# Performance work log

Measured on AMD Instinct MI355X. Metric: run time of the kernel, lower is better.

Reference implementation:

```python
import jax, jax.numpy as jnp
import numpy as np

EMBED_DIM = 1024
NUM_HEADS = 16
HEAD_DIM = EMBED_DIM // NUM_HEADS


def setup_inputs() -> dict:
    key = jax.random.key(0)
    k1, k2, k3, k4, k5 = jax.random.split(key, 5)
    B, N, C = 8, 1024, EMBED_DIM
    s = 1.0 / np.sqrt(C)
    return {
        "x": jax.random.normal(k1, (B, N, C), dtype=jnp.float32),
        "in_proj_weight": jax.random.normal(k2, (3 * C, C), dtype=jnp.float32) * s,
        "in_proj_bias": jax.random.normal(k3, (3 * C,), dtype=jnp.float32) * 0.02,
        "out_proj_weight": jax.random.normal(k4, (C, C), dtype=jnp.float32) * s,
        "out_proj_bias": jax.random.normal(k5, (C,), dtype=jnp.float32) * 0.02,
    }


def reference(x, in_proj_weight, in_proj_bias, out_proj_weight, out_proj_bias):
    B, N, C = x.shape
    scale = HEAD_DIM ** -0.5
    # qkv projection: F.linear(x, W, b) = x @ W.T + b -> [B, N, 3C]
    qkv = jnp.einsum("bnc,dc->bnd", x, in_proj_weight) + in_proj_bias
    # [B, N, 3, H, Dh] -> [3, B, H, N, Dh]
    qkv = qkv.reshape(B, N, 3, NUM_HEADS, HEAD_DIM).transpose(2, 0, 3, 1, 4)
    q, k, v = qkv[0], qkv[1], qkv[2]
    attn = jnp.einsum("bhqd,bhkd->bhqk", q, k) * scale
    attn = jax.nn.softmax(attn, axis=-1)
    out = jnp.einsum("bhqk,bhkd->bhqd", attn, v)
    out = out.transpose(0, 2, 1, 3).reshape(B, N, C)
    return jnp.einsum("bnc,dc->bnd", out, out_proj_weight) + out_proj_bias
```

## Files before the change

kernel.cpp:

```cpp
#include <hip/hip_runtime.h>
#include <math.h>
#include <stdint.h>

#define SEQ   1024
#define BATCH 8
#define CDIM  1024
#define HEADS 16
#define DHEAD 64

typedef __bf16 bf16;
typedef _Float16 f16;
typedef __attribute__((ext_vector_type(8))) _Float16 f16x8;
typedef __attribute__((ext_vector_type(4))) float f32x4;

static __device__ __forceinline__ void gl16(const void* g, void* l) {
    __builtin_amdgcn_global_load_lds(
        (const __attribute__((address_space(1))) void*)(uintptr_t)g,
        (__attribute__((address_space(3))) void*)(uintptr_t)l,
        16, 0, 0);
}

__global__ __launch_bounds__(256)
void cvt_f16(const float* __restrict__ in, f16* __restrict__ out, int n8)
{
    int i = blockIdx.x * blockDim.x + threadIdx.x;
    const int stride = gridDim.x * blockDim.x;
    for (; i < n8; i += stride) {
        const f32x4 v0 = *(const f32x4*)(in + (size_t)i * 8);
        const f32x4 v1 = *(const f32x4*)(in + (size_t)i * 8 + 4);
        f16x8 o;
#pragma unroll
        for (int j = 0; j < 4; j++) {
            o[j]     = (f16)v0[j];
            o[j + 4] = (f16)v1[j];
        }
        *(f16x8*)(out + (size_t)i * 8) = o;
    }
}

template<int MODE>
__global__ __launch_bounds__(256, 3)
void gemm_f16(const f16* __restrict__ Ag, const f16* __restrict__ Bg,
              const float* __restrict__ bias, float* __restrict__ out0,
              f16* __restrict__ qg, f16* __restrict__ kgp, f16* __restrict__ vgp,
              int M, int Ncols, int K)
{
    __shared__ f16 As[3][4][128][8];
    __shared__ f16 Bs[3][4][128][8];

    const int m0   = blockIdx.y * 128;
    const int n0   = blockIdx.x * 128;

    const int tid  = threadIdx.x;
    const int wid  = tid >> 6;
    const int lane = tid & 63;
    const int wr   = (wid >> 1) * 64;
    const int wc   = (wid & 1) * 64;
    const int l16  = lane & 15;
    const int kgf  = lane >> 4;

    const int kg0 = tid >> 7, row0 = tid & 127;
    const f16* aP = Ag + (size_t)(m0 + row0) * K + kg0 * 8;
    const f16* bP = Bg + (size_t)(n0 + row0) * K + kg0 * 8;
    const int loff = wid << 10;

#define STAGE(buf, kt)                                              \
    do {                                                            \
        gl16(aP + (kt),      (char*)&As[buf][0][0][0] + loff);      \
        gl16(aP + (kt) + 16, (char*)&As[buf][0][0][0] + loff + 4096);\
        gl16(bP + (kt),      (char*)&Bs[buf][0][0][0] + loff);      \
        gl16(bP + (kt) + 16, (char*)&Bs[buf][0][0][0] + loff + 4096);\
    } while (0)

#define COMPUTE(buf)                                                        \
    do {                                                                    \
        f16x8 fa[4], fb[4];                                                 \
        _Pragma("unroll")                                                   \
        for (int i = 0; i < 4; i++) {                                       \
            fa[i] = *(const f16x8*)&As[buf][kgf][wr + i * 16 + l16][0];     \
            fb[i] = *(const f16x8*)&Bs[buf][kgf][wc + i * 16 + l16][0];     \
        }                                                                   \
        _Pragma("unroll")                                                   \
        for (int mi = 0; mi < 4; mi++)                                      \
            _Pragma("unroll")                                               \
            for (int ni = 0; ni < 4; ni++)                                  \
                acc[mi][ni] = __builtin_amdgcn_mfma_f32_16x16x32_f16(       \
                    fa[mi], fb[ni], acc[mi][ni], 0, 0, 0);                  \
    } while (0)

    f32x4 acc[4][4];
#pragma unroll
    for (int i = 0; i < 4; i++)
#pragma unroll
        for (int j = 0; j < 4; j++) acc[i][j] = (f32x4)0.f;

    const int T = K >> 5;

    STAGE(0, 0);
    STAGE(1, 32);

    int cur = 0;
    for (int t = 0; t < T - 2; t++) {
        const int nbuf = (cur == 0) ? 2 : (cur - 1);
        STAGE(nbuf, (t + 2) << 5);
        asm volatile("s_waitcnt vmcnt(8)" ::: "memory");
        __builtin_amdgcn_sched_barrier(0);
        __builtin_amdgcn_s_barrier();
        __builtin_amdgcn_sched_barrier(0);
        COMPUTE(cur);
        __builtin_amdgcn_sched_barrier(0);
        __builtin_amdgcn_s_barrier();
        cur = (cur == 2) ? 0 : (cur + 1);
    }

    asm volatile("s_waitcnt vmcnt(4)" ::: "memory");
    __builtin_amdgcn_sched_barrier(0);
    __builtin_amdgcn_s_barrier();
    __builtin_amdgcn_sched_barrier(0);
    COMPUTE(cur);
    __builtin_amdgcn_sched_barrier(0);
    __builtin_amdgcn_s_barrier();
    cur = (cur == 2) ? 0 : (cur + 1);

    asm volatile("s_waitcnt vmcnt(0)" ::: "memory");
    __builtin_amdgcn_sched_barrier(0);
    __builtin_amdgcn_s_barrier();
    __builtin_amdgcn_sched_barrier(0);
    COMPUTE(cur);

#undef STAGE
#undef COMPUTE

#pragma unroll
    for (int ni = 0; ni < 4; ni++) {
        const int d  = n0 + wc + ni * 16 + l16;
        const float bv = bias[d];
        int s = 0, hh = 0, dh = 0;
        if (MODE == 1) {
            s  = d >> 10;
            hh = (d >> 6) & 15;
            dh = d & 63;
        }
#pragma unroll
        for (int mi = 0; mi < 4; mi++) {
            const int mbase = m0 + wr + mi * 16 + (lane >> 4) * 4;
#pragma unroll
            for (int r = 0; r < 4; r++) {
                const float v = acc[mi][ni][r] + bv;
                const int m = mbase + r;
                if (MODE == 0) {
                    out0[(size_t)m * Ncols + d] = v;
                } else {
                    const int b = m >> 10, n = m & 1023;
                    const size_t bho = (size_t)((b << 4) + hh) << 16;
                    if (s == 0)
                        qg[bho + ((size_t)n << 6) + dh] = (f16)(v * 0.125f);
                    else if (s == 1)
                        kgp[bho + ((size_t)n << 6) + dh] = (f16)v;
                    else
                        vgp[bho + ((size_t)dh << 10) + n] = (f16)v;
                }
            }
        }
    }
    (void)M;
}

__global__ __launch_bounds__(256, 4)
void attn_mfma(const f16* __restrict__ qf, const f16* __restrict__ kf,
               const f16* __restrict__ vtf, f16* __restrict__ og)
{
    __shared__ f16 Kl[8][64][8];
    __shared__ f16 Vl[8][64][8];
    __shared__ f16 Pl[4][16][72];

    const int tid  = threadIdx.x;
    const int wid  = tid >> 6;
    const int lane = tid & 63;
    const int l16  = lane & 15;
    const int kg   = lane >> 4;
    const int bh   = blockIdx.y;
    const int q0   = blockIdx.x << 6;

    const size_t bhoff = (size_t)bh << 16;
    const f16* qb = qf  + bhoff;
    const f16* kb = kf  + bhoff;
    const f16* vb = vtf + bhoff;

    f16x8 qfr[2];
    {
        const f16* qrow = qb + ((size_t)(q0 + wid * 16 + l16) << 6);
        qfr[0] = *(const f16x8*)(qrow + kg * 8);
        qfr[1] = *(const f16x8*)(qrow + 32 + kg * 8);
    }

    const int c0 = tid,        col0 = c0 & 63, slot0 = c0 >> 6;
    const int c1 = tid + 256,  col1 = c1 & 63, slot1 = c1 >> 6;

    float mrow[4], lrow[4];
    f32x4 accO[4];
#pragma unroll
    for (int r = 0; r < 4; r++) { mrow[r] = -INFINITY; lrow[r] = 0.f; }
#pragma unroll
    for (int t = 0; t < 4; t++) accO[t] = (f32x4)0.f;

    f16x8 rk0 = *(const f16x8*)(kb + ((size_t)col0 << 6) + slot0 * 8);
    f16x8 rk1 = *(const f16x8*)(kb + ((size_t)col1 << 6) + slot1 * 8);
    f16x8 rv0 = *(const f16x8*)(vb + ((size_t)col0 << 10) + slot0 * 8);
    f16x8 rv1 = *(const f16x8*)(vb + ((size_t)col1 << 10) + slot1 * 8);

    for (int kt = 0; kt < 16; kt++) {
        __syncthreads();
        *(f16x8*)&Kl[slot0][col0][0] = rk0;
        *(f16x8*)&Kl[slot1][col1][0] = rk1;
        *(f16x8*)&Vl[slot0][col0][0] = rv0;
        *(f16x8*)&Vl[slot1][col1][0] = rv1;
        __syncthreads();

        if (kt < 15) {
            const int n1 = (kt + 1) << 6;
            rk0 = *(const f16x8*)(kb + ((size_t)(n1 + col0) << 6) + slot0 * 8);
            rk1 = *(const f16x8*)(kb + ((size_t)(n1 + col1) << 6) + slot1 * 8);
            rv0 = *(const f16x8*)(vb + ((size_t)col0 << 10) + n1 + slot0 * 8);
            rv1 = *(const f16x8*)(vb + ((size_t)col1 << 10) + n1 + slot1 * 8);
        }

        f32x4 accS[4];
#pragma unroll
        for (int t = 0; t < 4; t++) accS[t] = (f32x4)0.f;
#pragma unroll
        for (int t = 0; t < 4; t++) {
            const f16x8 kf0 = *(const f16x8*)&Kl[kg][t * 16 + l16][0];
            const f16x8 kf1 = *(const f16x8*)&Kl[4 + kg][t * 16 + l16][0];
            accS[t] = __builtin_amdgcn_mfma_f32_16x16x32_f16(qfr[0], kf0, accS[t], 0, 0, 0);
            accS[t] = __builtin_amdgcn_mfma_f32_16x16x32_f16(qfr[1], kf1, accS[t], 0, 0, 0);
        }

#pragma unroll
        for (int r = 0; r < 4; r++) {
            float sm = fmaxf(fmaxf(accS[0][r], accS[1][r]),
                             fmaxf(accS[2][r], accS[3][r]));
            sm = fmaxf(sm, __shfl_xor(sm, 1, 16));
            sm = fmaxf(sm, __shfl_xor(sm, 2, 16));
            sm = fmaxf(sm, __shfl_xor(sm, 4, 16));
            sm = fmaxf(sm, __shfl_xor(sm, 8, 16));
            const float mn = fmaxf(mrow[r], sm);
            const float al = __expf(mrow[r] - mn);
            float p0 = __expf(accS[0][r] - mn);
            float p1 = __expf(accS[1][r] - mn);
            float p2 = __expf(accS[2][r] - mn);
            float p3 = __expf(accS[3][r] - mn);
            float rs = (p0 + p1) + (p2 + p3);
            rs += __shfl_xor(rs, 1, 16);
            rs += __shfl_xor(rs, 2, 16);
            rs += __shfl_xor(rs, 4, 16);
            rs += __shfl_xor(rs, 8, 16);
            lrow[r] = lrow[r] * al + rs;
            mrow[r] = mn;
            accO[0][r] *= al;
            accO[1][r] *= al;
            accO[2][r] *= al;
            accO[3][r] *= al;
            const int prow = kg * 4 + r;
            Pl[wid][prow][l16]      = (f16)p0;
            Pl[wid][prow][16 + l16] = (f16)p1;
            Pl[wid][prow][32 + l16] = (f16)p2;
            Pl[wid][prow][48 + l16] = (f16)p3;
        }

#pragma unroll
        for (int h = 0; h < 2; h++) {
            const f16x8 pa = *(const f16x8*)&Pl[wid][l16][h * 32 + kg * 8];
#pragma unroll
            for (int t = 0; t < 4; t++) {
                const f16x8 vf = *(const f16x8*)&Vl[h * 4 + kg][t * 16 + l16][0];
                accO[t] = __builtin_amdgcn_mfma_f32_16x16x32_f16(pa, vf, accO[t], 0, 0, 0);
            }
        }
    }

    const int b = bh >> 4, hh = bh & 15;
#pragma unroll
    for (int r = 0; r < 4; r++) {
        const float inv = 1.0f / lrow[r];
        const int n = q0 + wid * 16 + kg * 4 + r;
        const size_t base = ((((size_t)b << 10) + n) << 10) + hh * 64;
#pragma unroll
        for (int t = 0; t < 4; t++)
            og[base + t * 16 + l16] = (f16)(accO[t][r] * inv);
    }
}

#define TILE 128
#define KB   16
#define LSTR (TILE + 4)

template<int MODE>
__global__ __launch_bounds__(256, 2)
void gemm_bt(const float* __restrict__ A, const float* __restrict__ Bm,
             const float* __restrict__ bias, float* __restrict__ out0,
             float* __restrict__ qg, float* __restrict__ kg, float* __restrict__ vg,
             int M, int Ncols, int K)
{
    __shared__ float As[KB][LSTR];
    __shared__ float Bs[KB][LSTR];

    const int tid = threadIdx.x;
    const int tr  = tid >> 4;
    const int tc  = tid & 15;
    const int m0  = blockIdx.y * TILE;
    const int n0  = blockIdx.x * TILE;

    const int lrow = tid >> 2;
    const int lcol = (tid & 3) << 2;

    const float* Ap = A  + (size_t)(m0 + lrow) * K + lcol;
    const float* Bp = Bm + (size_t)(n0 + lrow) * K + lcol;
    const size_t rstep = (size_t)64 * K;

    float acc[8][8];
#pragma unroll
    for (int i = 0; i < 8; i++)
#pragma unroll
        for (int j = 0; j < 8; j++) acc[i][j] = 0.f;

    for (int kt = 0; kt < K; kt += KB) {
        float4 a0 = *(const float4*)(Ap + kt);
        float4 a1 = *(const float4*)(Ap + rstep + kt);
        float4 b0 = *(const float4*)(Bp + kt);
        float4 b1 = *(const float4*)(Bp + rstep + kt);
        __syncthreads();
        As[lcol + 0][lrow]      = a0.x;
        As[lcol + 1][lrow]      = a0.y;
        As[lcol + 2][lrow]      = a0.z;
        As[lcol + 3][lrow]      = a0.w;
        As[lcol + 0][lrow + 64] = a1.x;
        As[lcol + 1][lrow + 64] = a1.y;
        As[lcol + 2][lrow + 64] = a1.z;
        As[lcol + 3][lrow + 64] = a1.w;
        Bs[lcol + 0][lrow]      = b0.x;
        Bs[lcol + 1][lrow]      = b0.y;
        Bs[lcol + 2][lrow]      = b0.z;
        Bs[lcol + 3][lrow]      = b0.w;
        Bs[lcol + 0][lrow + 64] = b1.x;
        Bs[lcol + 1][lrow + 64] = b1.y;
        Bs[lcol + 2][lrow + 64] = b1.z;
        Bs[lcol + 3][lrow + 64] = b1.w;
        __syncthreads();
#pragma unroll
        for (int kk = 0; kk < KB; kk++) {
            float ar[8], br[8];
            *(float4*)&ar[0] = *(const float4*)&As[kk][tr << 2];
            *(float4*)&ar[4] = *(const float4*)&As[kk][64 + (tr << 2)];
            *(float4*)&br[0] = *(const float4*)&Bs[kk][tc << 2];
            *(float4*)&br[4] = *(const float4*)&Bs[kk][64 + (tc << 2)];
#pragma unroll
            for (int i = 0; i < 8; i++)
#pragma unroll
                for (int j = 0; j < 8; j++)
                    acc[i][j] = fmaf(ar[i], br[j], acc[i][j]);
        }
    }

#pragma unroll
    for (int rg = 0; rg < 2; rg++) {
#pragma unroll
        for (int ri = 0; ri < 4; ri++) {
            const int m = m0 + rg * 64 + (tr << 2) + ri;
#pragma unroll
            for (int cg = 0; cg < 2; cg++) {
                const int d = n0 + cg * 64 + (tc << 2);
                const float4 bb = *(const float4*)&bias[d];
                float v0 = acc[rg * 4 + ri][cg * 4 + 0] + bb.x;
                float v1 = acc[rg * 4 + ri][cg * 4 + 1] + bb.y;
                float v2 = acc[rg * 4 + ri][cg * 4 + 2] + bb.z;
                float v3 = acc[rg * 4 + ri][cg * 4 + 3] + bb.w;
                if (MODE == 0) {
                    *(float4*)&out0[(size_t)m * Ncols + d] = make_float4(v0, v1, v2, v3);
                } else {
                    const int s  = d >> 10;
                    const int h  = (d >> 6) & 15;
                    const int dh = d & 63;
                    const int b  = m >> 10;
                    const int n  = m & 1023;
                    float* dst = (s == 0) ? qg : ((s == 1) ? kg : vg);
                    if (s == 0) { v0 *= 0.125f; v1 *= 0.125f; v2 *= 0.125f; v3 *= 0.125f; }
                    const size_t idx = (((size_t)((b << 4) + h) << 10) + n) * 64 + dh;
                    *(float4*)&dst[idx] = make_float4(v0, v1, v2, v3);
                }
            }
        }
    }
}

__global__ __launch_bounds__(256, 2)
void attn_flash_f32(const float* __restrict__ qg, const float* __restrict__ kg,
                    const float* __restrict__ vg, float* __restrict__ og)
{
    __shared__ float Qs[64][68];
    __shared__ float KPs[64][68];
    __shared__ float Vs[64][68];

    const int tid = threadIdx.x;
    const int tr  = tid >> 4;
    const int tc  = tid & 15;
    const int bh  = blockIdx.y;
    const int q0  = blockIdx.x << 6;

    const float* qb = qg + ((size_t)bh * SEQ + q0) * DHEAD;
    const float* kb = kg + (size_t)bh * SEQ * DHEAD;
    const float* vb = vg + (size_t)bh * SEQ * DHEAD;

    const int lr = tid >> 4;
    const int lc = (tid & 15) << 2;

#pragma unroll
    for (int i = 0; i < 4; i++) {
        const int r = lr + (i << 4);
        float4 t = *(const float4*)(qb + r * 64 + lc);
        Qs[lc + 0][r] = t.x;
        Qs[lc + 1][r] = t.y;
        Qs[lc + 2][r] = t.z;
        Qs[lc + 3][r] = t.w;
    }

    float m[4], l[4], acc[4][4];
#pragma unroll
    for (int i = 0; i < 4; i++) {
        m[i] = -INFINITY; l[i] = 0.f;
#pragma unroll
        for (int j = 0; j < 4; j++) acc[i][j] = 0.f;
    }

    for (int kt = 0; kt < 16; kt++) {
        __syncthreads();
        const float* kbt = kb + (size_t)(kt << 6) * 64;
        const float* vbt = vb + (size_t)(kt << 6) * 64;
#pragma unroll
        for (int i = 0; i < 4; i++) {
            const int r = lr + (i << 4);
            float4 t = *(const float4*)(kbt + r * 64 + lc);
            KPs[lc + 0][r] = t.x;
            KPs[lc + 1][r] = t.y;
            KPs[lc + 2][r] = t.z;
            KPs[lc + 3][r] = t.w;
            float4 tv = *(const float4*)(vbt + r * 64 + lc);
            *(float4*)&Vs[r][lc] = tv;
        }
        __syncthreads();

        float s[4][4];
#pragma unroll
        for (int i = 0; i < 4; i++)
#pragma unroll
            for (int j = 0; j < 4; j++) s[i][j] = 0.f;
#pragma unroll 4
        for (int d = 0; d < 64; d++) {
            float qa[4], ka[4];
            *(float4*)qa = *(const float4*)&Qs[d][tr << 2];
            *(float4*)ka = *(const float4*)&KPs[d][tc << 2];
#pragma unroll
            for (int ri = 0; ri < 4; ri++)
#pragma unroll
                for (int ci = 0; ci < 4; ci++)
                    s[ri][ci] = fmaf(qa[ri], ka[ci], s[ri][ci]);
        }
        __syncthreads();

#pragma unroll
        for (int ri = 0; ri < 4; ri++) {
            float tm = fmaxf(fmaxf(s[ri][0], s[ri][1]), fmaxf(s[ri][2], s[ri][3]));
            tm = fmaxf(tm, __shfl_xor(tm, 1, 16));
            tm = fmaxf(tm, __shfl_xor(tm, 2, 16));
            tm = fmaxf(tm, __shfl_xor(tm, 4, 16));
            tm = fmaxf(tm, __shfl_xor(tm, 8, 16));
            const float mn = fmaxf(m[ri], tm);
            const float alpha = __expf(m[ri] - mn);
            const float p0 = __expf(s[ri][0] - mn);
            const float p1 = __expf(s[ri][1] - mn);
            const float p2 = __expf(s[ri][2] - mn);
            const float p3 = __expf(s[ri][3] - mn);
            float rs = (p0 + p1) + (p2 + p3);
            rs += __shfl_xor(rs, 1, 16);
            rs += __shfl_xor(rs, 2, 16);
            rs += __shfl_xor(rs, 4, 16);
            rs += __shfl_xor(rs, 8, 16);
            l[ri] = l[ri] * alpha + rs;
            m[ri] = mn;
            acc[ri][0] *= alpha; acc[ri][1] *= alpha;
            acc[ri][2] *= alpha; acc[ri][3] *= alpha;
            *(float4*)&KPs[(tr << 2) + ri][tc << 2] = make_float4(p0, p1, p2, p3);
        }
        __syncthreads();

#pragma unroll 4
        for (int c = 0; c < 64; c += 4) {
            float pr[4][4], vv[4][4];
            *(float4*)pr[0] = *(const float4*)&KPs[(tr << 2) + 0][c];
            *(float4*)pr[1] = *(const float4*)&KPs[(tr << 2) + 1][c];
            *(float4*)pr[2] = *(const float4*)&KPs[(tr << 2) + 2][c];
            *(float4*)pr[3] = *(const float4*)&KPs[(tr << 2) + 3][c];
            *(float4*)vv[0] = *(const float4*)&Vs[c + 0][tc << 2];
            *(float4*)vv[1] = *(const float4*)&Vs[c + 1][tc << 2];
            *(float4*)vv[2] = *(const float4*)&Vs[c + 2][tc << 2];
            *(float4*)vv[3] = *(const float4*)&Vs[c + 3][tc << 2];
#pragma unroll
            for (int ri = 0; ri < 4; ri++)
#pragma unroll
                for (int j = 0; j < 4; j++) {
                    float a = acc[ri][j];
                    a = fmaf(pr[ri][0], vv[0][j], a);
                    a = fmaf(pr[ri][1], vv[1][j], a);
                    a = fmaf(pr[ri][2], vv[2][j], a);
                    a = fmaf(pr[ri][3], vv[3][j], a);
                    acc[ri][j] = a;
                }
        }
    }

    const int b = bh >> 4, h = bh & 15;
#pragma unroll
    for (int ri = 0; ri < 4; ri++) {
        const float inv = 1.0f / l[ri];
        const int n = q0 + (tr << 2) + ri;
        const size_t idx = (((size_t)b * SEQ + n) << 10) + (h << 6) + (tc << 2);
        *(float4*)&og[idx] = make_float4(acc[ri][0] * inv, acc[ri][1] * inv,
                                         acc[ri][2] * inv, acc[ri][3] * inv);
    }
}

extern "C" void kernel_launch(void* const* d_in, const int* in_sizes, int n_in,
                              void* d_out, int out_size, void* d_ws, size_t ws_size,
                              hipStream_t stream)
{
    const float* x     = (const float*)d_in[0];
    const float* w_in  = (const float*)d_in[1];
    const float* b_in  = (const float*)d_in[2];
    const float* w_out = (const float*)d_in[3];
    const float* b_out = (const float*)d_in[4];
    float* out = (float*)d_out;
    (void)in_sizes; (void)n_in; (void)out_size;

    const size_t MB  = 1024 * 1024;
    const size_t per = (size_t)BATCH * HEADS * SEQ * DHEAD;
    const int    M   = BATCH * SEQ;
    char* ws = (char*)d_ws;

    if (ws_size >= 96 * MB) {
        f16* qf16  = (f16*)(ws + 0 * MB);
        f16* kf16  = (f16*)(ws + 16 * MB);
        f16* vtf16 = (f16*)(ws + 32 * MB);
        f16* xf16  = (f16*)(ws + 48 * MB);
        f16* of16  = xf16;
        f16* wif16 = (f16*)(ws + 64 * MB);
        f16* wof16 = (f16*)(ws + 70 * MB);

        cvt_f16<<<2048, 256, 0, stream>>>(x,     xf16,  (int)(per / 8));
        cvt_f16<<<1024, 256, 0, stream>>>(w_in,  wif16, 3 * CDIM * CDIM / 8);
        cvt_f16<<<512,  256, 0, stream>>>(w_out, wof16, CDIM * CDIM / 8);

        gemm_f16<1><<<dim3(3 * CDIM / 128, M / 128), 256, 0, stream>>>(
            xf16, wif16, b_in, nullptr, qf16, kf16, vtf16, M, 3 * CDIM, CDIM);

        attn_mfma<<<dim3(SEQ / 64, BATCH * HEADS), 256, 0, stream>>>(
            qf16, kf16, vtf16, of16);

        gemm_f16<0><<<dim3(CDIM / 128, M / 128), 256, 0, stream>>>(
            of16, wof16, b_out, out, nullptr, nullptr, nullptr, M, CDIM, CDIM);
    } else {
        float* qws = (float*)d_ws;
        float* kws = qws + per;
        float* vws = kws + per;
        float* aws = vws + per;

        gemm_bt<1><<<dim3(3 * CDIM / TILE, M / TILE), 256, 0, stream>>>(
            x, w_in, b_in, nullptr, qws, kws, vws, M, 3 * CDIM, CDIM);

        attn_flash_f32<<<dim3(SEQ / 64, BATCH * HEADS), 256, 0, stream>>>(
            qws, kws, vws, aws);

        gemm_bt<0><<<dim3(CDIM / TILE, M / TILE), 256, 0, stream>>>(
            aws, w_out, b_out, out, nullptr, nullptr, nullptr, M, CDIM, CDIM);
    }
}
```

Measured before the change: 286.9 us.

## Add 256x256-tile 8-wave QKV GEMM with interleaved prefetch and MFMA phases

Replaces the 128x128 QKV projection GEMM with a new kernel using 256x256 tiles, 512 threads (8 waves each computing 128x64), double-buffered LDS fed by direct global-to-LDS loads, and the K-step split into four phases that interleave prefetch issue with MFMA bursts under explicit barriers and raised wave priority. The larger tile raises arithmetic intensity and cuts global traffic per FLOP. The cost is heavy register use for 32 accumulators, 128KB LDS per block, and only 384 blocks for the grid, which may leave CUs underfilled. The epilogue still scatters Q (pre-scaled), K and transposed V with scalar f16 stores.

After: 281.4 us. No clear change (-1.9%).

```diff
diff --git a/kernel.cpp b/kernel.cpp
--- a/kernel.cpp
+++ b/kernel.cpp
@@ -35,6 +35,174 @@
             o[j + 4] = (f16)v1[j];
         }
         *(f16x8*)(out + (size_t)i * 8) = o;
+    }
+}
+
+__global__ __launch_bounds__(512, 2)
+void gemm_qkv8(const f16* __restrict__ Ag, const f16* __restrict__ Bg,
+               const float* __restrict__ bias,
+               f16* __restrict__ qg, f16* __restrict__ kgp, f16* __restrict__ vgp,
+               int K)
+{
+    __shared__ f16 As[2][8][256][8];
+    __shared__ f16 Bs[2][8][256][8];
+
+    const int tid  = threadIdx.x;
+    const int wid  = tid >> 6;
+    const int lane = tid & 63;
+    const int wrow = (wid >> 2) << 7;
+    const int wcol = (wid & 3) << 6;
+    const int l16  = lane & 15;
+    const int kgf  = lane >> 4;
+    const int m0   = blockIdx.y << 8;
+    const int n0   = blockIdx.x << 8;
+
+    const int srow = tid & 255;
+    const int sks0 = tid >> 8;
+    const int sldq = (tid & 192) << 4;
+
+    const f16* aP = Ag + (size_t)(m0 + srow) * K + sks0 * 8;
+    const f16* bP = Bg + (size_t)(n0 + srow) * K + sks0 * 8;
+    char* AsB = (char*)&As[0][0][0][0];
+    char* BsB = (char*)&Bs[0][0][0][0];
+
+#define SA(bb, tt, j) gl16(aP + ((tt) << 6) + ((j) << 4), \
+        AsB + (bb) * 32768 + ((sks0 + 2 * (j)) << 12) + sldq)
+#define SB(bb, tt, j) gl16(bP + ((tt) << 6) + ((j) << 4), \
+        BsB + (bb) * 32768 + ((sks0 + 2 * (j)) << 12) + sldq)
+
+    f32x4 acc[8][4];
+#pragma unroll
+    for (int i = 0; i < 8; i++)
+#pragma unroll
+        for (int j = 0; j < 4; j++) acc[i][j] = (f32x4)0.f;
+
+    const int T = K >> 6;
+
+    SA(0, 0, 0); SA(0, 0, 1);
+    SB(0, 0, 0); SB(0, 0, 1);
+    SA(0, 0, 2); SA(0, 0, 3);
+    SB(0, 0, 2); SB(0, 0, 3);
+    asm volatile("s_waitcnt vmcnt(4)" ::: "memory");
+    __builtin_amdgcn_sched_barrier(0);
+    __builtin_amdgcn_s_barrier();
+
+    int buf = 0;
+    for (int t = 0; t < T; t++) {
+        const int nb = buf ^ 1;
+        const int tn = (t + 1 == T) ? 0 : (t + 1);
+
+        f16x8 fa[4], fb[4];
+
+#pragma unroll
+        for (int j = 0; j < 4; j++)
+            fb[j] = *(const f16x8*)&Bs[buf][kgf][wcol + j * 16 + l16][0];
+#pragma unroll
+        for (int i = 0; i < 4; i++)
+            fa[i] = *(const f16x8*)&As[buf][kgf][wrow + i * 16 + l16][0];
+        SA(nb, tn, 0); SA(nb, tn, 1);
+        __builtin_amdgcn_s_barrier();
+        asm volatile("s_waitcnt lgkmcnt(0)" ::: "memory");
+        __builtin_amdgcn_sched_barrier(0);
+        __builtin_amdgcn_s_setprio(1);
+#pragma unroll
+        for (int i = 0; i < 4; i++)
+#pragma unroll
+            for (int j = 0; j < 4; j++)
+                acc[i][j] = __builtin_amdgcn_mfma_f32_16x16x32_f16(
+                    fa[i], fb[j], acc[i][j], 0, 0, 0);
+        __builtin_amdgcn_s_setprio(0);
+        __builtin_amdgcn_s_barrier();
+
+#pragma unroll
+        for (int i = 0; i < 4; i++)
+            fa[i] = *(const f16x8*)&As[buf][kgf][wrow + (i + 4) * 16 + l16][0];
+        SB(nb, tn, 0); SB(nb, tn, 1);
+        asm volatile("s_waitcnt vmcnt(4)" ::: "memory");
+        __builtin_amdgcn_sched_barrier(0);
+        __builtin_amdgcn_s_barrier();
+        asm volatile("s_waitcnt lgkmcnt(0)" ::: "memory");
+        __builtin_amdgcn_sched_barrier(0);
+        __builtin_amdgcn_s_setprio(1);
+#pragma unroll
+        for (int i = 0; i < 4; i++)
+#pragma unroll
+            for (int j = 0; j < 4; j++)
+                acc[i + 4][j] = __builtin_amdgcn_mfma_f32_16x16x32_f16(
+                    fa[i], fb[j], acc[i + 4][j], 0, 0, 0);
+        __builtin_amdgcn_s_setprio(0);
+        __builtin_amdgcn_s_barrier();
+
+#pragma unroll
+        for (int j = 0; j < 4; j++)
+            fb[j] = *(const f16x8*)&Bs[buf][4 + kgf][wcol + j * 16 + l16][0];
+#pragma unroll
+        for (int i = 0; i < 4; i++)
+            fa[i] = *(const f16x8*)&As[buf][4 + kgf][wrow + i * 16 + l16][0];
+        SA(nb, tn, 2); SA(nb, tn, 3);
+        __builtin_amdgcn_s_barrier();
+        asm volatile("s_waitcnt lgkmcnt(0)" ::: "memory");
+        __builtin_amdgcn_sched_barrier(0);
+        __builtin_amdgcn_s_setprio(1);
+#pragma unroll
+        for (int i = 0; i < 4; i++)
+#pragma unroll
+            for (int j = 0; j < 4; j++)
+                acc[i][j] = __builtin_amdgcn_mfma_f32_16x16x32_f16(
+                    fa[i], fb[j], acc[i][j], 0, 0, 0);
+        __builtin_amdgcn_s_setprio(0);
+        __builtin_amdgcn_s_barrier();
+
+#pragma unroll
+        for (int i = 0; i < 4; i++)
+            fa[i] = *(const f16x8*)&As[buf][4 + kgf][wrow + (i + 4) * 16 + l16][0];
+        SB(nb, tn, 2); SB(nb, tn, 3);
+        asm volatile("s_waitcnt vmcnt(4)" ::: "memory");
+        __builtin_amdgcn_sched_barrier(0);
+        __builtin_amdgcn_s_barrier();
+        asm volatile("s_waitcnt lgkmcnt(0)" ::: "memory");
+        __builtin_amdgcn_sched_barrier(0);
+        __builtin_amdgcn_s_setprio(1);
+#pragma unroll
+        for (int i = 0; i < 4; i++)
+#pragma unroll
+            for (int j = 0; j < 4; j++)
+                acc[i + 4][j] = __builtin_amdgcn_mfma_f32_16x16x32_f16(
+                    fa[i], fb[j], acc[i + 4][j], 0, 0, 0);
+        __builtin_amdgcn_s_setprio(0);
+        __builtin_amdgcn_s_barrier();
+
+        buf = nb;
+    }
+    asm volatile("s_waitcnt vmcnt(0)" ::: "memory");
+    __builtin_amdgcn_sched_barrier(0);
+#undef SA
+#undef SB
+
+#pragma unroll
+    for (int j = 0; j < 4; j++) {
+        const int d  = n0 + wcol + j * 16 + l16;
+        const float bv = bias[d];
+        const int s  = d >> 10;
+        const int hh = (d >> 6) & 15;
+        const int dh = d & 63;
+#pragma unroll
+        for (int i = 0; i < 8; i++) {
+            const int mbase = m0 + wrow + i * 16 + (lane >> 4) * 4;
+#pragma unroll
+            for (int r = 0; r < 4; r++) {
+                const float v = acc[i][j][r] + bv;
+                const int m = mbase + r;
+                const int b = m >> 10, n = m & 1023;
+                const size_t bho = (size_t)((b << 4) + hh) << 16;
+                if (s == 0)
+                    qg[bho + ((size_t)n << 6) + dh] = (f16)(v * 0.125f);
+                else if (s == 1)
+                    kgp[bho + ((size_t)n << 6) + dh] = (f16)v;
+                else
+                    vgp[bho + ((size_t)dh << 10) + n] = (f16)v;
+            }
+        }
     }
 }
 
@@ -559,8 +727,8 @@
         cvt_f16<<<1024, 256, 0, stream>>>(w_in,  wif16, 3 * CDIM * CDIM / 8);
         cvt_f16<<<512,  256, 0, stream>>>(w_out, wof16, CDIM * CDIM / 8);
 
-        gemm_f16<1><<<dim3(3 * CDIM / 128, M / 128), 256, 0, stream>>>(
-            xf16, wif16, b_in, nullptr, qf16, kf16, vtf16, M, 3 * CDIM, CDIM);
+        gemm_qkv8<<<dim3(3 * CDIM / 256, M / 256), 512, 0, stream>>>(
+            xf16, wif16, b_in, qf16, kf16, vtf16, CDIM);
 
         attn_mfma<<<dim3(SEQ / 64, BATCH * HEADS), 256, 0, stream>>>(
             qf16, kf16, vtf16, of16);
```

## Merge f16 conversion kernels and widen QKV GEMM tile to 128x256

Applied to the files above, without the earlier changes.

Replaces the three separate fp32-to-f16 conversion launches with one kernel that walks x, the input weight and the output weight in a single grid. Replaces the templated QKV GEMM with a dedicated 128x256 tile variant in which each wave computes a 64x128 sub-tile, using triple-buffered global-to-LDS loads. The wider tile raises operand reuse per loaded A row and halves the number of blocks, at the cost of more accumulator registers and LDS, which lowers occupancy to 2 blocks per CU. The Q scaling by 0.125 is folded into the epilogue.

After: 271.7 us. -5.3%, faster.

```diff
diff --git a/kernel.cpp b/kernel.cpp
--- a/kernel.cpp
+++ b/kernel.cpp
@@ -21,20 +21,150 @@
 }
 
 __global__ __launch_bounds__(256)
-void cvt_f16(const float* __restrict__ in, f16* __restrict__ out, int n8)
+void cvt_all(const float* __restrict__ x,  const float* __restrict__ wi,
+             const float* __restrict__ wo, f16* __restrict__ xo,
+             f16* __restrict__ wio, f16* __restrict__ woo)
 {
+    const int N1 = 1048576, N2 = 393216;
+    const int NT = N1 + N2 + 131072;
     int i = blockIdx.x * blockDim.x + threadIdx.x;
     const int stride = gridDim.x * blockDim.x;
-    for (; i < n8; i += stride) {
-        const f32x4 v0 = *(const f32x4*)(in + (size_t)i * 8);
-        const f32x4 v1 = *(const f32x4*)(in + (size_t)i * 8 + 4);
+    for (; i < NT; i += stride) {
+        const float* src; f16* dst; int off;
+        if (i < N1)            { src = x;  dst = xo;  off = i; }
+        else if (i < N1 + N2)  { src = wi; dst = wio; off = i - N1; }
+        else                   { src = wo; dst = woo; off = i - N1 - N2; }
+        const f32x4 v0 = *(const f32x4*)(src + (size_t)off * 8);
+        const f32x4 v1 = *(const f32x4*)(src + (size_t)off * 8 + 4);
         f16x8 o;
 #pragma unroll
         for (int j = 0; j < 4; j++) {
             o[j]     = (f16)v0[j];
             o[j + 4] = (f16)v1[j];
         }
-        *(f16x8*)(out + (size_t)i * 8) = o;
+        *(f16x8*)(dst + (size_t)off * 8) = o;
+    }
+}
+
+__global__ __launch_bounds__(256, 2)
+void gemm_qkv_wide(const f16* __restrict__ Ag, const f16* __restrict__ Bg,
+                   const float* __restrict__ bias,
+                   f16* __restrict__ qg, f16* __restrict__ kgp,
+                   f16* __restrict__ vgp, int K)
+{
+    __shared__ f16 As[3][4][128][8];
+    __shared__ f16 Bs[3][4][256][8];
+
+    const int m0 = blockIdx.y * 128;
+    const int n0 = blockIdx.x * 256;
+
+    const int tid  = threadIdx.x;
+    const int wid  = tid >> 6;
+    const int lane = tid & 63;
+    const int wr   = (wid >> 1) * 64;
+    const int wc   = (wid & 1) * 128;
+    const int l16  = lane & 15;
+    const int kgf  = lane >> 4;
+
+    const int akg = tid >> 7, arow = tid & 127;
+    const f16* aP = Ag + (size_t)(m0 + arow) * K + akg * 8;
+    const f16* bP = Bg + (size_t)(n0 + tid) * K;
+    const int loff = wid << 10;
+
+#define STAGE(buf, kt)                                               \
+    do {                                                             \
+        gl16(aP + (kt),      (char*)As[buf] + loff);                 \
+        gl16(aP + (kt) + 16, (char*)As[buf] + loff + 4096);          \
+        gl16(bP + (kt),      (char*)Bs[buf] + loff);                 \
+        gl16(bP + (kt) + 8,  (char*)Bs[buf] + loff + 4096);         \
+        gl16(bP + (kt) + 16, (char*)Bs[buf] + loff + 8192);         \
+        gl16(bP + (kt) + 24, (char*)Bs[buf] + loff + 12288);        \
+    } while (0)
+
+#define COMPUTE(buf)                                                         \
+    do {                                                                     \
+        f16x8 fa[4], fb[8];                                                  \
+        _Pragma("unroll")                                                    \
+        for (int i = 0; i < 4; i++)                                          \
+            fa[i] = *(const f16x8*)&As[buf][kgf][wr + i * 16 + l16][0];      \
+        _Pragma("unroll")                                                    \
+        for (int j = 0; j < 8; j++)                                          \
+            fb[j] = *(const f16x8*)&Bs[buf][kgf][wc + j * 16 + l16][0];      \
+        _Pragma("unroll")                                                    \
+        for (int i = 0; i < 4; i++)                                          \
+            _Pragma("unroll")                                                \
+            for (int j = 0; j < 8; j++)                                      \
+                acc[i][j] = __builtin_amdgcn_mfma_f32_16x16x32_f16(          \
+                    fa[i], fb[j], acc[i][j], 0, 0, 0);                       \
+    } while (0)
+
+    f32x4 acc[4][8];
+#pragma unroll
+    for (int i = 0; i < 4; i++)
+#pragma unroll
+        for (int j = 0; j < 8; j++) acc[i][j] = (f32x4)0.f;
+
+    const int T = K >> 5;
+
+    STAGE(0, 0);
+    STAGE(1, 32);
+
+    int cur = 0;
+    for (int t = 0; t < T - 2; t++) {
+        const int nbuf = (cur == 0) ? 2 : (cur - 1);
+        STAGE(nbuf, (t + 2) << 5);
+        asm volatile("s_waitcnt vmcnt(12)" ::: "memory");
+        __builtin_amdgcn_sched_barrier(0);
+        __builtin_amdgcn_s_barrier();
+        __builtin_amdgcn_sched_barrier(0);
+        COMPUTE(cur);
+        __builtin_amdgcn_sched_barrier(0);
+        __builtin_amdgcn_s_barrier();
+        cur = (cur == 2) ? 0 : (cur + 1);
+    }
+
+    asm volatile("s_waitcnt vmcnt(6)" ::: "memory");
+    __builtin_amdgcn_sched_barrier(0);
+    __builtin_amdgcn_s_barrier();
+    __builtin_amdgcn_sched_barrier(0);
+    COMPUTE(cur);
+    __builtin_amdgcn_sched_barrier(0);
+    __builtin_amdgcn_s_barrier();
+    cur = (cur == 2) ? 0 : (cur + 1);
+
+    asm volatile("s_waitcnt vmcnt(0)" ::: "memory");
+    __builtin_amdgcn_sched_barrier(0);
+    __builtin_amdgcn_s_barrier();
+    __builtin_amdgcn_sched_barrier(0);
+    COMPUTE(cur);
+
+#undef STAGE
+#undef COMPUTE
+
+#pragma unroll
+    for (int j = 0; j < 8; j++) {
+        const int d  = n0 + wc + j * 16 + l16;
+        const float bv = bias[d];
+        const int s  = d >> 10;
+        const int hh = (d >> 6) & 15;
+        const int dh = d & 63;
+#pragma unroll
+        for (int i = 0; i < 4; i++) {
+            const int mbase = m0 + wr + i * 16 + (lane >> 4) * 4;
+#pragma unroll
+            for (int r = 0; r < 4; r++) {
+                const float v = acc[i][j][r] + bv;
+                const int m = mbase + r;
+                const int b = m >> 10, n = m & 1023;
+                const size_t bho = (size_t)((b << 4) + hh) << 16;
+                if (s == 0)
+                    qg[bho + ((size_t)n << 6) + dh] = (f16)(v * 0.125f);
+                else if (s == 1)
+                    kgp[bho + ((size_t)n << 6) + dh] = (f16)v;
+                else
+                    vgp[bho + ((size_t)dh << 10) + n] = (f16)v;
+            }
+        }
     }
 }
 
@@ -555,12 +685,10 @@
         f16* wif16 = (f16*)(ws + 64 * MB);
         f16* wof16 = (f16*)(ws + 70 * MB);
 
-        cvt_f16<<<2048, 256, 0, stream>>>(x,     xf16,  (int)(per / 8));
-        cvt_f16<<<1024, 256, 0, stream>>>(w_in,  wif16, 3 * CDIM * CDIM / 8);
-        cvt_f16<<<512,  256, 0, stream>>>(w_out, wof16, CDIM * CDIM / 8);
-
-        gemm_f16<1><<<dim3(3 * CDIM / 128, M / 128), 256, 0, stream>>>(
-            xf16, wif16, b_in, nullptr, qf16, kf16, vtf16, M, 3 * CDIM, CDIM);
+        cvt_all<<<1536, 256, 0, stream>>>(x, w_in, w_out, xf16, wif16, wof16);
+
+        gemm_qkv_wide<<<dim3(3 * CDIM / 256, M / 128), 256, 0, stream>>>(
+            xf16, wif16, b_in, qf16, kf16, vtf16, CDIM);
 
         attn_mfma<<<dim3(SEQ / 64, BATCH * HEADS), 256, 0, stream>>>(
             qf16, kf16, vtf16, of16);
```
